# Optimization experiments

Measured on AMD Instinct MI355X. Metric: run time of the kernel, lower is better.

## Reference

```python
import jax, jax.numpy as jnp
import numpy as np

N_CELLS, IN_DIM, HID, OUT = 65536, 128, 256, 128
MLP_H = 128   # engine MLP hidden width is hard-coded to 128 in the source
N_MORPH = 32  # min(32, n_cells//4)


def setup_inputs() -> dict:
    key = jax.random.key(0)
    ks = jax.random.split(key, 18)
    s = 0.05
    return {
        "x": jax.random.normal(ks[0], (1, IN_DIM), jnp.float32),
        "hiddens": jax.random.normal(ks[1], (N_CELLS, HID), jnp.float32) * 0.1,
        "Wa1": jax.random.normal(ks[2], (MLP_H, IN_DIM + HID), jnp.float32) * s,
        "ba1": jax.random.normal(ks[3], (MLP_H,), jnp.float32) * s,
        "Wa2": jax.random.normal(ks[4], (OUT, MLP_H), jnp.float32) * s,
        "ba2": jax.random.normal(ks[5], (OUT,), jnp.float32) * s,
        "Wg1": jax.random.normal(ks[6], (MLP_H, IN_DIM + HID), jnp.float32) * s,
        "bg1": jax.random.normal(ks[7], (MLP_H,), jnp.float32) * s,
        "Wg2": jax.random.normal(ks[8], (OUT, MLP_H), jnp.float32) * s,
        "bg2": jax.random.normal(ks[9], (OUT,), jnp.float32) * s,
        "W_ih": jax.random.normal(ks[10], (3 * HID, OUT + 1), jnp.float32) * s,
        "W_hh": jax.random.normal(ks[11], (3 * HID, HID), jnp.float32) * s,
        "b_ih": jax.random.normal(ks[12], (3 * HID,), jnp.float32) * s,
        "b_hh": jax.random.normal(ks[13], (3 * HID,), jnp.float32) * s,
        "nat_w": jnp.eye(HID, dtype=jnp.float32),  # nn.init.eye_
        "morph_w": jax.random.normal(ks[14], (N_MORPH, HID, HID), jnp.float32) * 0.02,
        "morph_src": jax.random.randint(ks[15], (N_MORPH,), 0, N_CELLS, jnp.int32),
        "morph_tgt": jax.random.randint(ks[16], (N_MORPH,), 0, N_CELLS, jnp.int32),
        "step": 0,
    }


def _forward(x, hiddens, Wa1, ba1, Wa2, ba2, Wg1, bg1, Wg2, bg2,
             W_ih, W_hh, b_ih, b_hh, nat_w, morph_w, morph_src, morph_tgt, step):
    n = hiddens.shape[0]
    # --- BenchMind, batched over all cells (x broadcast to every cell) ---
    xb = jnp.broadcast_to(x, (n, x.shape[-1]))
    combined = jnp.concatenate([xb, hiddens], axis=-1)               # [n, in+hid]
    a = jax.nn.relu(combined @ Wa1.T + ba1) @ Wa2.T + ba2            # [n, out]
    g = jax.nn.relu(combined @ Wg1.T + bg1) @ Wg2.T + bg2            # [n, out]
    out = a - g                                                       # [n, out]
    tension = jnp.mean(out * out, axis=-1, keepdims=True)            # [n, 1]
    # mem_input is detached in torch
    mem_in = jax.lax.stop_gradient(jnp.concatenate([out, tension], axis=-1))
    # --- PyTorch GRUCell math ---
    gi = mem_in @ W_ih.T + b_ih                                      # [n, 3H]
    gh = hiddens @ W_hh.T + b_hh                                     # [n, 3H]
    i_r, i_z, i_n = jnp.split(gi, 3, axis=-1)
    h_r, h_z, h_n = jnp.split(gh, 3, axis=-1)
    r = jax.nn.sigmoid(i_r + h_r)
    z = jax.nn.sigmoid(i_z + h_z)
    nn_ = jnp.tanh(i_n + r * h_n)
    hid = jax.lax.stop_gradient((1.0 - z) * nn_ + z * hiddens)       # detached new hiddens
    if step % 3 == 0:
        hid = jax.lax.stop_gradient(hid @ nat_w.T)                   # natural transformation
    # --- limit / colimit (morphism gather-transform-aggregate) ---
    limit = jnp.einsum('mij,mj->i', morph_w, hid[morph_src]) / N_MORPH
    colimit = jnp.einsum('mji,mj->i', morph_w, hid[morph_tgt]) / N_MORPH
    diff = limit - colimit
    cat_tension = jnp.mean(diff * diff)
    hid = hid + 0.05 * jax.lax.stop_gradient(diff)[None, :]
    # --- faction sync (+ debate if step > 5) ---
    n_f = min(8, n // 2)
    fs = n // n_f
    hf = hid[: n_f * fs].reshape(n_f, fs, hid.shape[-1])
    fmean = hf.mean(axis=1, keepdims=True)                           # [n_f,1,H]
    hf = 0.85 * hf + 0.15 * fmean
    if step > 5:
        global_op = hf.mean(axis=1).mean(axis=0)                     # mean of faction means
        dc = max(1, fs // 4)
        hf = hf.at[:, :dc].set(0.85 * hf[:, :dc] + 0.15 * global_op)
    hid = jnp.concatenate([hf.reshape(n_f * fs, -1), hid[n_f * fs:]], axis=0)
    # --- tension-weighted combination (weights detached: .item() in torch) ---
    t = jax.lax.stop_gradient(tension[:, 0])                         # [n]
    w = jax.nn.softmax(t, axis=0)
    combined_out = jnp.sum(w[:, None] * out, axis=0, keepdims=True)  # [1, out]
    avg_tension = jnp.mean(tension) + 0.1 * cat_tension
    return combined_out, avg_tension, hid


def reference(x, hiddens, Wa1, ba1, Wa2, ba2, Wg1, bg1, Wg2, bg2,
              W_ih, W_hh, b_ih, b_hh, nat_w, morph_w, morph_src, morph_tgt, step):
    combined_out, avg_tension, _ = _forward(
        x, hiddens, Wa1, ba1, Wa2, ba2, Wg1, bg1, Wg2, bg2,
        W_ih, W_hh, b_ih, b_hh, nat_w, morph_w, morph_src, morph_tgt, step)
    return combined_out, avg_tension
```

## Files before the change

### kernel.cpp

```cpp
#include <hip/hip_runtime.h>
#include <math.h>

#define OFF_W1B   0
#define OFF_W2A   32768
#define OFF_XW1B  49152
#define OFF_B2D   49408
#define OFF_PT    49536
#define OFF_PE    51584
#define OFF_POUT  53632
#define OFF_MI4   315776
#define OFF_TEN   323968
#define OFF_HH4   324032
#define OFF_GI    340416
#define OFF_GH    389568
#define OFF_PLIM  438720
#define OFF_PCOL8 446912
#define OFF_GMSK  512448

typedef short bf16x8 __attribute__((ext_vector_type(8)));
typedef short s16x4  __attribute__((ext_vector_type(4)));
typedef float f32x4  __attribute__((ext_vector_type(4)));

__device__ __forceinline__ unsigned short f2bf(float f) {
    unsigned u = __builtin_bit_cast(unsigned, f);
    u += 0x7FFFu + ((u >> 16) & 1u);
    return (unsigned short)(u >> 16);
}

__device__ __forceinline__ bf16x8 cvt8(float4 a, float4 b) {
    bf16x8 v;
    v[0] = (short)f2bf(a.x); v[1] = (short)f2bf(a.y);
    v[2] = (short)f2bf(a.z); v[3] = (short)f2bf(a.w);
    v[4] = (short)f2bf(b.x); v[5] = (short)f2bf(b.y);
    v[6] = (short)f2bf(b.z); v[7] = (short)f2bf(b.w);
    return v;
}

__global__ __launch_bounds__(256) void k_prep(
    const float* __restrict__ x, const float* __restrict__ hiddens,
    const float* __restrict__ Wa1, const float* __restrict__ ba1,
    const float* __restrict__ Wa2, const float* __restrict__ ba2,
    const float* __restrict__ Wg1, const float* __restrict__ bg1,
    const float* __restrict__ Wg2, const float* __restrict__ bg2,
    const int* __restrict__ msrc, const int* __restrict__ mtgt,
    float* __restrict__ ws)
{
    const int b = blockIdx.x, t = threadIdx.x;
    unsigned short* w1b = (unsigned short*)(ws + OFF_W1B);
    unsigned short* w2a = (unsigned short*)(ws + OFF_W2A);
    if (b < 256) {
        const int n = b;
        const float* row = (n < 128) ? &Wa1[n * 384] : &Wg1[(n - 128) * 384];
        const int kc = t >> 3;
        w1b[(kc * 256 + n) * 8 + (t & 7)] = f2bf(row[128 + t]);
        if (n < 128) {
            float w2 = (t < 128) ? Wa2[n * 128 + t] : -Wg2[n * 128 + (t - 128)];
            w2a[(kc * 128 + n) * 8 + (t & 7)] = f2bf(w2);
        }
    } else if (b == 256) {
        const int n = t;
        const float* wr = (n < 128) ? &Wa1[n * 384] : &Wg1[(n - 128) * 384];
        float s = (n < 128) ? ba1[n] : bg1[n - 128];
        for (int j = 0; j < 128; ++j) s = fmaf(x[j], wr[j], s);
        ws[OFF_XW1B + n] = s;
        if (n < 128) ws[OFF_B2D + n] = ba2[n] - bg2[n];
    } else if (b == 257) {
        unsigned* gm = (unsigned*)(ws + OFF_GMSK);
        for (int i = t; i < 2048; i += 256) gm[i] = 0u;
        __syncthreads();
        if (t < 64) {
            const int cell = (t < 32) ? msrc[t] : mtgt[t - 32];
            atomicOr(&gm[cell >> 5], 1u << (cell & 31));
        }
    } else {
        const int g = b - 258;
        const int cell = (g < 32) ? msrc[g] : mtgt[g - 32];
        ws[OFF_HH4 + (t >> 2) * 256 + g * 4 + (t & 3)] = hiddens[(size_t)cell * 256 + t];
    }
}

__global__ __launch_bounds__(256, 4) void k_main(
    const float* __restrict__ hiddens,
    const int* __restrict__ msrc, const int* __restrict__ mtgt,
    float* __restrict__ ws)
{
    __shared__ __align__(16) short hB[32 * 256];
    __shared__ __align__(16) short h1B[32 * 256];
    __shared__ float part[128];
    __shared__ float e_sm[32], t_sm_[32];
    __shared__ int gid_sm[64];

    const int tid  = threadIdx.x;
    const int lane = tid & 63, wid = tid >> 6;
    const int l15 = lane & 15, l4 = lane >> 4;
    const int blk = blockIdx.x;

    if (tid < 64) gid_sm[tid] = (tid < 32) ? msrc[tid] : mtgt[tid - 32];

    const uint4* w1g = (const uint4*)(ws + OFF_W1B);
    const uint4* w2g = (const uint4*)(ws + OFF_W2A);
    const unsigned* gm = (const unsigned*)(ws + OFF_GMSK);

    const int rc = tid >> 3;
    const int cb = (tid & 7) * 32;
    const float* hsrc0 = hiddens + (size_t)(blk * 64 + rc) * 256 + cb;

    float4 nx[8];
#pragma unroll
    for (int it = 0; it < 8; ++it) nx[it] = *(const float4*)(hsrc0 + it * 4);
#pragma unroll
    for (int it = 0; it < 4; ++it) {
        const int kc = (tid & 7) * 4 + it;
        *(bf16x8*)&hB[rc * 256 + ((kc ^ (rc & 15)) << 3)] = cvt8(nx[2 * it], nx[2 * it + 1]);
    }
    __syncthreads();

#pragma unroll
    for (int t = 0; t < 2; ++t) {
        const int bt = blk * 2 + t;

        uint4 wc[4], wn1[4], wn2[4];
#pragma unroll
        for (int q = 0; q < 4; ++q) {
            wc[q]  = w1g[(0 + l4) * 256 + wid * 64 + q * 16 + l15];
            wn1[q] = w1g[(4 + l4) * 256 + wid * 64 + q * 16 + l15];
        }
        uint4 g2c[2], g2n1[2];
        f32x4 acc[4][2];
#pragma unroll
        for (int q = 0; q < 4; ++q)
#pragma unroll
            for (int ct = 0; ct < 2; ++ct) acc[q][ct] = (f32x4)0.f;

        __builtin_amdgcn_s_setprio(1);
#pragma unroll
        for (int s = 0; s < 8; ++s) {
            if (s < 6) {
#pragma unroll
                for (int q = 0; q < 4; ++q)
                    wn2[q] = w1g[((s + 2) * 4 + l4) * 256 + wid * 64 + q * 16 + l15];
            } else if (s == 6) {
#pragma unroll
                for (int q = 0; q < 2; ++q)
                    g2c[q] = w2g[(0 + l4) * 128 + wid * 32 + q * 16 + l15];
            } else {
#pragma unroll
                for (int q = 0; q < 2; ++q)
                    g2n1[q] = w2g[(4 + l4) * 128 + wid * 32 + q * 16 + l15];
            }
            bf16x8 bfr[2];
#pragma unroll
            for (int ct = 0; ct < 2; ++ct) {
                const int c = ct * 16 + l15;
                bfr[ct] = *(const bf16x8*)&hB[c * 256 + (((s * 4 + l4) ^ l15) << 3)];
            }
#pragma unroll
            for (int q = 0; q < 4; ++q) {
                const bf16x8 af = __builtin_bit_cast(bf16x8, wc[q]);
                acc[q][0] = __builtin_amdgcn_mfma_f32_16x16x32_bf16(af, bfr[0], acc[q][0], 0, 0, 0);
                acc[q][1] = __builtin_amdgcn_mfma_f32_16x16x32_bf16(af, bfr[1], acc[q][1], 0, 0, 0);
            }
#pragma unroll
            for (int q = 0; q < 4; ++q) { wc[q] = wn1[q]; wn1[q] = wn2[q]; }
        }
        __builtin_amdgcn_s_setprio(0);

#pragma unroll
        for (int nt = 0; nt < 4; ++nt) {
            const int n0 = wid * 64 + nt * 16 + l4 * 4;
            float4 xb = *(const float4*)(ws + OFF_XW1B + n0);
            const float bx[4] = {xb.x, xb.y, xb.z, xb.w};
            const int chunk = n0 >> 3;
            const int off = (l4 & 1) * 4;
#pragma unroll
            for (int ct = 0; ct < 2; ++ct) {
                const int c = ct * 16 + l15;
                s16x4 pk;
#pragma unroll
                for (int r = 0; r < 4; ++r)
                    pk[r] = (short)f2bf(fmaxf(acc[nt][ct][r] + bx[r], 0.f));
                *(s16x4*)&h1B[c * 256 + ((chunk ^ l15) << 3) + off] = pk;
            }
        }
        __syncthreads();

        f32x4 acc2[2][2];
#pragma unroll
        for (int ot = 0; ot < 2; ++ot)
#pragma unroll
            for (int ct = 0; ct < 2; ++ct) acc2[ot][ct] = (f32x4)0.f;

        uint4 g2n2[2];
        __builtin_amdgcn_s_setprio(1);
#pragma unroll
        for (int s = 0; s < 8; ++s) {
            if (s < 6) {
#pragma unroll
                for (int q = 0; q < 2; ++q)
                    g2n2[q] = w2g[((s + 2) * 4 + l4) * 128 + wid * 32 + q * 16 + l15];
            }
            if (s == 5 && t == 0) {
#pragma unroll
                for (int it = 0; it < 8; ++it)
                    nx[it] = *(const float4*)(hsrc0 + 32 * 256 + it * 4);
            }
            bf16x8 b2[2];
#pragma unroll
            for (int ct = 0; ct < 2; ++ct) {
                const int c = ct * 16 + l15;
                b2[ct] = *(const bf16x8*)&h1B[c * 256 + (((s * 4 + l4) ^ l15) << 3)];
            }
#pragma unroll
            for (int ot = 0; ot < 2; ++ot) {
                const bf16x8 af = __builtin_bit_cast(bf16x8, g2c[ot]);
                acc2[ot][0] = __builtin_amdgcn_mfma_f32_16x16x32_bf16(af, b2[0], acc2[ot][0], 0, 0, 0);
                acc2[ot][1] = __builtin_amdgcn_mfma_f32_16x16x32_bf16(af, b2[1], acc2[ot][1], 0, 0, 0);
            }
#pragma unroll
            for (int q = 0; q < 2; ++q) { g2c[q] = g2n1[q]; g2n1[q] = g2n2[q]; }
        }
        __builtin_amdgcn_s_setprio(0);

        float outv[2][2][4];
#pragma unroll
        for (int ot = 0; ot < 2; ++ot) {
            float4 bd = *(const float4*)(ws + OFF_B2D + wid * 32 + ot * 16 + l4 * 4);
            const float bv[4] = {bd.x, bd.y, bd.z, bd.w};
#pragma unroll
            for (int ct = 0; ct < 2; ++ct)
#pragma unroll
                for (int r = 0; r < 4; ++r)
                    outv[ot][ct][r] = acc2[ot][ct][r] + bv[r];
        }

#pragma unroll
        for (int ct = 0; ct < 2; ++ct) {
            float sq = 0.f;
#pragma unroll
            for (int ot = 0; ot < 2; ++ot)
#pragma unroll
                for (int r = 0; r < 4; ++r)
                    sq = fmaf(outv[ot][ct][r], outv[ot][ct][r], sq);
            sq += __shfl_xor(sq, 16);
            sq += __shfl_xor(sq, 32);
            if (l4 == 0) part[wid * 32 + ct * 16 + l15] = sq;
        }
        __syncthreads();

        if (tid < 32) {
            float s = part[tid] + part[32 + tid] + part[64 + tid] + part[96 + tid];
            const float tv = s * (1.f / 128.f);
            const float ev = expf(tv);
            t_sm_[tid] = tv; e_sm[tid] = ev;
            float pt = tv, pe = ev;
            for (int off = 16; off > 0; off >>= 1) {
                pt += __shfl_down(pt, off);
                pe += __shfl_down(pe, off);
            }
            if (tid == 0) { ws[OFF_PT + bt] = pt; ws[OFF_PE + bt] = pe; }
            unsigned m = gm[bt];
            while (m) {
                const int g = __builtin_ctz(m); m &= m - 1;
                const int cg = gid_sm[g];
                if ((cg >> 5) == bt && (cg & 31) == tid) ws[OFF_TEN + g] = tv;
            }
        }
        __syncthreads();

        {
            float p[2][4];
#pragma unroll
            for (int ot = 0; ot < 2; ++ot)
#pragma unroll
                for (int r = 0; r < 4; ++r) {
                    float s = e_sm[l15] * outv[ot][0][r];
                    s = fmaf(e_sm[16 + l15], outv[ot][1][r], s);
                    p[ot][r] = s;
                }
#pragma unroll
            for (int ot = 0; ot < 2; ++ot)
#pragma unroll
                for (int r = 0; r < 4; ++r) {
                    p[ot][r] += __shfl_xor(p[ot][r], 1);
                    p[ot][r] += __shfl_xor(p[ot][r], 2);
                    p[ot][r] += __shfl_xor(p[ot][r], 4);
                    p[ot][r] += __shfl_xor(p[ot][r], 8);
                }
            if (l15 == 0) {
#pragma unroll
                for (int ot = 0; ot < 2; ++ot)
                    *(float4*)(ws + OFF_POUT + (size_t)bt * 128 + wid * 32 + ot * 16 + l4 * 4) =
                        make_float4(p[ot][0], p[ot][1], p[ot][2], p[ot][3]);
            }
        }
        {
            unsigned m = gm[bt];
            while (m) {
                const int g = __builtin_ctz(m); m &= m - 1;
                const int cg = gid_sm[g];
                if ((cg >> 5) != bt) continue;
                const int c = cg & 31;
                if ((c & 15) == l15) {
                    const int ct = c >> 4;
#pragma unroll
                    for (int ot = 0; ot < 2; ++ot)
                        *(float4*)(ws + OFF_MI4 + (wid * 8 + ot * 4 + l4) * 256 + g * 4) =
                            make_float4(outv[ot][ct][0], outv[ot][ct][1],
                                        outv[ot][ct][2], outv[ot][ct][3]);
                }
            }
        }
        if (t == 0) {
#pragma unroll
            for (int it = 0; it < 4; ++it) {
                const int kc = (tid & 7) * 4 + it;
                *(bf16x8*)&hB[rc * 256 + ((kc ^ (rc & 15)) << 3)] = cvt8(nx[2 * it], nx[2 * it + 1]);
            }
            __syncthreads();
        }
    }
}

__global__ __launch_bounds__(256) void k_tail1(
    const float* __restrict__ W_ih, const float* __restrict__ W_hh,
    const float* __restrict__ b_ih, const float* __restrict__ b_hh,
    float* __restrict__ ws)
{
    const int lane = threadIdx.x & 63;
    const int w    = threadIdx.x >> 6;
    const int row  = __builtin_amdgcn_readfirstlane(blockIdx.x * 4 + w);
    const float* mi4 = ws + OFF_MI4;
    const float* hh4 = ws + OFF_HH4;

    const float* wi = W_ih + row * 129;
    float gi = b_ih[row];
#pragma unroll 8
    for (int q = 0; q < 32; ++q) {
        float4 a = *(const float4*)(mi4 + q * 256 + lane * 4);
        gi = fmaf(wi[4 * q + 0], a.x, gi);
        gi = fmaf(wi[4 * q + 1], a.y, gi);
        gi = fmaf(wi[4 * q + 2], a.z, gi);
        gi = fmaf(wi[4 * q + 3], a.w, gi);
    }
    gi = fmaf(ws[OFF_TEN + lane], wi[128], gi);

    const float* wh = W_hh + (size_t)row * 256;
    float gh = b_hh[row];
#pragma unroll 8
    for (int q = 0; q < 64; ++q) {
        float4 a = *(const float4*)(hh4 + q * 256 + lane * 4);
        float4 b = *(const float4*)(wh + 4 * q);
        gh = fmaf(b.x, a.x, gh);
        gh = fmaf(b.y, a.y, gh);
        gh = fmaf(b.z, a.z, gh);
        gh = fmaf(b.w, a.w, gh);
    }
    ws[OFF_GI + lane * 768 + row] = gi;
    ws[OFF_GH + lane * 768 + row] = gh;
}

__global__ __launch_bounds__(256) void k_morph(
    const float* __restrict__ morph_w, const float* __restrict__ nat_w,
    const int* __restrict__ step, float* __restrict__ ws)
{
    __shared__ float wsm[32 * 264];
    __shared__ float hd0[256], hd1[256];
    __shared__ float hs[256], ht[256];
    const int blk = blockIdx.x, t = threadIdx.x;
    const int m = blk >> 3, ch = blk & 7;
    const float* wm = morph_w + (size_t)m * 65536 + (size_t)ch * 32 * 256;
    {
        const int r = t >> 3, c0 = (t & 7) * 32;
#pragma unroll
        for (int it = 0; it < 8; ++it)
            *(float4*)&wsm[r * 264 + c0 + it * 4] = *(const float4*)(wm + r * 256 + c0 + it * 4);
    }
#pragma unroll
    for (int h = 0; h < 2; ++h) {
        const int g = h * 32 + m;
        const float i_r = ws[OFF_GI + g * 768 + t];
        const float i_z = ws[OFF_GI + g * 768 + 256 + t];
        const float i_n = ws[OFF_GI + g * 768 + 512 + t];
        const float h_r = ws[OFF_GH + g * 768 + t];
        const float h_z = ws[OFF_GH + g * 768 + 256 + t];
        const float h_n = ws[OFF_GH + g * 768 + 512 + t];
        const float hv  = ws[OFF_HH4 + (t >> 2) * 256 + g * 4 + (t & 3)];
        const float r  = 1.f / (1.f + expf(-(i_r + h_r)));
        const float z  = 1.f / (1.f + expf(-(i_z + h_z)));
        const float nn = tanhf(i_n + r * h_n);
        const float hid = (1.f - z) * nn + z * hv;
        if (h == 0) hd0[t] = hid; else hd1[t] = hid;
    }
    __syncthreads();

    float hn0, hn1;
    if (step[0] % 3 == 0) {
        const float4* wr = (const float4*)(nat_w + (size_t)t * 256);
        float s0 = 0.f, s1 = 0.f;
        for (int q = 0; q < 64; ++q) {
            float4 wq = wr[q];
            s0 = fmaf(wq.x, hd0[4 * q + 0], s0); s1 = fmaf(wq.x, hd1[4 * q + 0], s1);
            s0 = fmaf(wq.y, hd0[4 * q + 1], s0); s1 = fmaf(wq.y, hd1[4 * q + 1], s1);
            s0 = fmaf(wq.z, hd0[4 * q + 2], s0); s1 = fmaf(wq.z, hd1[4 * q + 2], s1);
            s0 = fmaf(wq.w, hd0[4 * q + 3], s0); s1 = fmaf(wq.w, hd1[4 * q + 3], s1);
        }
        hn0 = s0; hn1 = s1;
    } else {
        hn0 = hd0[t]; hn1 = hd1[t];
    }
    hs[t] = hn0; ht[t] = hn1;
    __syncthreads();

    {
        const int il = t >> 3, jc = t & 7;
        float L = 0.f;
#pragma unroll 8
        for (int jj = 0; jj < 32; ++jj) {
            const int j = jc + 8 * jj;
            L = fmaf(wsm[il * 264 + j], hs[j], L);
        }
        L += __shfl_down(L, 4);
        L += __shfl_down(L, 2);
        L += __shfl_down(L, 1);
        if (jc == 0) ws[OFF_PLIM + m * 256 + ch * 32 + il] = L;
    }
    {
        float C = 0.f;
#pragma unroll 8
        for (int r = 0; r < 32; ++r)
            C = fmaf(wsm[r * 264 + t], ht[ch * 32 + r], C);
        ws[OFF_PCOL8 + blk * 256 + t] = C;
    }
}

__global__ __launch_bounds__(256) void k_out(const float* __restrict__ ws,
                                             float* __restrict__ out)
{
    __shared__ float red[256];
    const int b = blockIdx.x, t = threadIdx.x;
    if (b < 128) {
        float so = 0.f, se = 0.f;
        for (int i = t; i < 2048; i += 256) {
            so += ws[OFF_POUT + (size_t)i * 128 + b];
            se += ws[OFF_PE + i];
        }
        red[t] = so; __syncthreads();
        for (int s = 128; s > 0; s >>= 1) { if (t < s) red[t] += red[t + s]; __syncthreads(); }
        const float SO = red[0]; __syncthreads();
        red[t] = se; __syncthreads();
        for (int s = 128; s > 0; s >>= 1) { if (t < s) red[t] += red[t + s]; __syncthreads(); }
        if (t == 0) out[b] = SO / red[0];
    } else {
        float pt = 0.f;
        for (int i = t; i < 2048; i += 256) pt += ws[OFF_PT + i];
        float L = 0.f, C = 0.f;
        for (int m = 0; m < 32; ++m) L += ws[OFF_PLIM + m * 256 + t];
        for (int mc = 0; mc < 256; ++mc) C += ws[OFF_PCOL8 + mc * 256 + t];
        const float d = (L - C) * (1.f / 32.f);
        red[t] = d * d; __syncthreads();
        for (int s = 128; s > 0; s >>= 1) { if (t < s) red[t] += red[t + s]; __syncthreads(); }
        const float cat = red[0] * (1.f / 256.f); __syncthreads();
        red[t] = pt; __syncthreads();
        for (int s = 128; s > 0; s >>= 1) { if (t < s) red[t] += red[t + s]; __syncthreads(); }
        if (t == 0) out[128] = red[0] * (1.f / 65536.f) + 0.1f * cat;
    }
}

extern "C" void kernel_launch(void* const* d_in, const int* in_sizes, int n_in,
                              void* d_out, int out_size, void* d_ws, size_t ws_size,
                              hipStream_t stream)
{
    const float* x     = (const float*)d_in[0];
    const float* hidd  = (const float*)d_in[1];
    const float* Wa1   = (const float*)d_in[2];
    const float* ba1   = (const float*)d_in[3];
    const float* Wa2   = (const float*)d_in[4];
    const float* ba2   = (const float*)d_in[5];
    const float* Wg1   = (const float*)d_in[6];
    const float* bg1   = (const float*)d_in[7];
    const float* Wg2   = (const float*)d_in[8];
    const float* bg2   = (const float*)d_in[9];
    const float* W_ih  = (const float*)d_in[10];
    const float* W_hh  = (const float*)d_in[11];
    const float* b_ih  = (const float*)d_in[12];
    const float* b_hh  = (const float*)d_in[13];
    const float* nat_w = (const float*)d_in[14];
    const float* mw    = (const float*)d_in[15];
    const int*   msrc  = (const int*)d_in[16];
    const int*   mtgt  = (const int*)d_in[17];
    const int*   step  = (const int*)d_in[18];

    float* out = (float*)d_out;
    float* ws  = (float*)d_ws;

    k_prep <<<322, 256, 0, stream>>>(x, hidd, Wa1, ba1, Wa2, ba2, Wg1, bg1, Wg2, bg2, msrc, mtgt, ws);
    k_main <<<1024, 256, 0, stream>>>(hidd, msrc, mtgt, ws);
    k_tail1<<<192, 256, 0, stream>>>(W_ih, W_hh, b_ih, b_hh, ws);
    k_morph<<<256, 256, 0, stream>>>(mw, nat_w, step, ws);
    k_out  <<<129, 256, 0, stream>>>(ws, out);
}
```

Baseline: 82.63 us.

## Process one 32-cell tile per block and drop cross-tile hidden-state prefetch

The main kernel now handles a single 32-cell tile per block and launches twice as many blocks, instead of looping over two tiles per block with a software prefetch of the second tile's hidden rows during the first tile's second GEMM. The launch-bounds occupancy hint drops from 4 to 2 blocks per CU, and the unrolled weight prefetch is written with scalar variables. This gives up intra-block overlap of global loads with MFMA work and relies on more resident blocks to hide latency. Each block also reloads the weight fragments itself, so the per-block setup cost is paid twice as often.

```diff
diff --git a/kernel.cpp b/kernel.cpp
--- a/kernel.cpp
+++ b/kernel.cpp
@@ -79,7 +79,7 @@
     }
 }
 
-__global__ __launch_bounds__(256, 4) void k_main(
+__global__ __launch_bounds__(256, 2) void k_main(
     const float* __restrict__ hiddens,
     const int* __restrict__ msrc, const int* __restrict__ mtgt,
     float* __restrict__ ws)
@@ -93,7 +93,7 @@
     const int tid  = threadIdx.x;
     const int lane = tid & 63, wid = tid >> 6;
     const int l15 = lane & 15, l4 = lane >> 4;
-    const int blk = blockIdx.x;
+    const int bt = blockIdx.x;
 
     if (tid < 64) gid_sm[tid] = (tid < 32) ? msrc[tid] : mtgt[tid - 32];
 
@@ -101,222 +101,204 @@
     const uint4* w2g = (const uint4*)(ws + OFF_W2A);
     const unsigned* gm = (const unsigned*)(ws + OFF_GMSK);
 
-    const int rc = tid >> 3;
-    const int cb = (tid & 7) * 32;
-    const float* hsrc0 = hiddens + (size_t)(blk * 64 + rc) * 256 + cb;
-
-    float4 nx[8];
-#pragma unroll
-    for (int it = 0; it < 8; ++it) nx[it] = *(const float4*)(hsrc0 + it * 4);
-#pragma unroll
-    for (int it = 0; it < 4; ++it) {
-        const int kc = (tid & 7) * 4 + it;
-        *(bf16x8*)&hB[rc * 256 + ((kc ^ (rc & 15)) << 3)] = cvt8(nx[2 * it], nx[2 * it + 1]);
-    }
-    __syncthreads();
-
-#pragma unroll
-    for (int t = 0; t < 2; ++t) {
-        const int bt = blk * 2 + t;
-
-        uint4 wc[4], wn1[4], wn2[4];
-#pragma unroll
-        for (int q = 0; q < 4; ++q) {
-            wc[q]  = w1g[(0 + l4) * 256 + wid * 64 + q * 16 + l15];
-            wn1[q] = w1g[(4 + l4) * 256 + wid * 64 + q * 16 + l15];
-        }
-        uint4 g2c[2], g2n1[2];
-        f32x4 acc[4][2];
-#pragma unroll
-        for (int q = 0; q < 4; ++q)
-#pragma unroll
-            for (int ct = 0; ct < 2; ++ct) acc[q][ct] = (f32x4)0.f;
-
-        __builtin_amdgcn_s_setprio(1);
-#pragma unroll
-        for (int s = 0; s < 8; ++s) {
-            if (s < 6) {
-#pragma unroll
-                for (int q = 0; q < 4; ++q)
-                    wn2[q] = w1g[((s + 2) * 4 + l4) * 256 + wid * 64 + q * 16 + l15];
-            } else if (s == 6) {
-#pragma unroll
-                for (int q = 0; q < 2; ++q)
-                    g2c[q] = w2g[(0 + l4) * 128 + wid * 32 + q * 16 + l15];
-            } else {
-#pragma unroll
-                for (int q = 0; q < 2; ++q)
-                    g2n1[q] = w2g[(4 + l4) * 128 + wid * 32 + q * 16 + l15];
+    {
+        const int rc = tid >> 3;
+        const float* hsrc = hiddens + (size_t)(bt * 32 + rc) * 256 + (tid & 7) * 32;
+        float4 v0 = *(const float4*)(hsrc + 0);
+        float4 v1 = *(const float4*)(hsrc + 4);
+        float4 v2 = *(const float4*)(hsrc + 8);
+        float4 v3 = *(const float4*)(hsrc + 12);
+        float4 v4 = *(const float4*)(hsrc + 16);
+        float4 v5 = *(const float4*)(hsrc + 20);
+        float4 v6 = *(const float4*)(hsrc + 24);
+        float4 v7 = *(const float4*)(hsrc + 28);
+        const int kc0 = (tid & 7) * 4;
+        *(bf16x8*)&hB[rc * 256 + (((kc0 + 0) ^ (rc & 15)) << 3)] = cvt8(v0, v1);
+        *(bf16x8*)&hB[rc * 256 + (((kc0 + 1) ^ (rc & 15)) << 3)] = cvt8(v2, v3);
+        *(bf16x8*)&hB[rc * 256 + (((kc0 + 2) ^ (rc & 15)) << 3)] = cvt8(v4, v5);
+        *(bf16x8*)&hB[rc * 256 + (((kc0 + 3) ^ (rc & 15)) << 3)] = cvt8(v6, v7);
+    }
+    __syncthreads();
+
+    const int wb1 = wid * 64 + l15;
+    uint4 c0 = w1g[(0 + l4) * 256 + wb1 + 0];
+    uint4 c1 = w1g[(0 + l4) * 256 + wb1 + 16];
+    uint4 c2 = w1g[(0 + l4) * 256 + wb1 + 32];
+    uint4 c3 = w1g[(0 + l4) * 256 + wb1 + 48];
+    uint4 p0 = w1g[(4 + l4) * 256 + wb1 + 0];
+    uint4 p1 = w1g[(4 + l4) * 256 + wb1 + 16];
+    uint4 p2 = w1g[(4 + l4) * 256 + wb1 + 32];
+    uint4 p3 = w1g[(4 + l4) * 256 + wb1 + 48];
+    uint4 g2c0, g2c1, g2p0, g2p1;
+
+    f32x4 acc[4][2];
+#pragma unroll
+    for (int q = 0; q < 4; ++q)
+#pragma unroll
+        for (int ct = 0; ct < 2; ++ct) acc[q][ct] = (f32x4)0.f;
+
+    __builtin_amdgcn_s_setprio(1);
+#pragma unroll
+    for (int s = 0; s < 8; ++s) {
+        uint4 f0, f1, f2, f3;
+        if (s < 6) {
+            f0 = w1g[((s + 2) * 4 + l4) * 256 + wb1 + 0];
+            f1 = w1g[((s + 2) * 4 + l4) * 256 + wb1 + 16];
+            f2 = w1g[((s + 2) * 4 + l4) * 256 + wb1 + 32];
+            f3 = w1g[((s + 2) * 4 + l4) * 256 + wb1 + 48];
+        } else if (s == 6) {
+            g2c0 = w2g[(0 + l4) * 128 + wid * 32 + l15];
+            g2c1 = w2g[(0 + l4) * 128 + wid * 32 + 16 + l15];
+        } else {
+            g2p0 = w2g[(4 + l4) * 128 + wid * 32 + l15];
+            g2p1 = w2g[(4 + l4) * 128 + wid * 32 + 16 + l15];
+        }
+        bf16x8 bfr0 = *(const bf16x8*)&hB[(0 * 16 + l15) * 256 + (((s * 4 + l4) ^ l15) << 3)];
+        bf16x8 bfr1 = *(const bf16x8*)&hB[(1 * 16 + l15) * 256 + (((s * 4 + l4) ^ l15) << 3)];
+        acc[0][0] = __builtin_amdgcn_mfma_f32_16x16x32_bf16(__builtin_bit_cast(bf16x8, c0), bfr0, acc[0][0], 0, 0, 0);
+        acc[0][1] = __builtin_amdgcn_mfma_f32_16x16x32_bf16(__builtin_bit_cast(bf16x8, c0), bfr1, acc[0][1], 0, 0, 0);
+        acc[1][0] = __builtin_amdgcn_mfma_f32_16x16x32_bf16(__builtin_bit_cast(bf16x8, c1), bfr0, acc[1][0], 0, 0, 0);
+        acc[1][1] = __builtin_amdgcn_mfma_f32_16x16x32_bf16(__builtin_bit_cast(bf16x8, c1), bfr1, acc[1][1], 0, 0, 0);
+        acc[2][0] = __builtin_amdgcn_mfma_f32_16x16x32_bf16(__builtin_bit_cast(bf16x8, c2), bfr0, acc[2][0], 0, 0, 0);
+        acc[2][1] = __builtin_amdgcn_mfma_f32_16x16x32_bf16(__builtin_bit_cast(bf16x8, c2), bfr1, acc[2][1], 0, 0, 0);
+        acc[3][0] = __builtin_amdgcn_mfma_f32_16x16x32_bf16(__builtin_bit_cast(bf16x8, c3), bfr0, acc[3][0], 0, 0, 0);
+        acc[3][1] = __builtin_amdgcn_mfma_f32_16x16x32_bf16(__builtin_bit_cast(bf16x8, c3), bfr1, acc[3][1], 0, 0, 0);
+        c0 = p0; c1 = p1; c2 = p2; c3 = p3;
+        if (s < 6) { p0 = f0; p1 = f1; p2 = f2; p3 = f3; }
+    }
+    __builtin_amdgcn_s_setprio(0);
+
+#pragma unroll
+    for (int nt = 0; nt < 4; ++nt) {
+        const int n0 = wid * 64 + nt * 16 + l4 * 4;
+        float4 xb = *(const float4*)(ws + OFF_XW1B + n0);
+        const float bx[4] = {xb.x, xb.y, xb.z, xb.w};
+        const int chunk = n0 >> 3;
+        const int off = (l4 & 1) * 4;
+#pragma unroll
+        for (int ct = 0; ct < 2; ++ct) {
+            const int c = ct * 16 + l15;
+            s16x4 pk;
+#pragma unroll
+            for (int r = 0; r < 4; ++r)
+                pk[r] = (short)f2bf(fmaxf(acc[nt][ct][r] + bx[r], 0.f));
+            *(s16x4*)&h1B[c * 256 + ((chunk ^ l15) << 3) + off] = pk;
+        }
+    }
+    __syncthreads();
+
+    f32x4 acc2[2][2];
+#pragma unroll
+    for (int ot = 0; ot < 2; ++ot)
+#pragma unroll
+        for (int ct = 0; ct < 2; ++ct) acc2[ot][ct] = (f32x4)0.f;
+
+    __builtin_amdgcn_s_setprio(1);
+#pragma unroll
+    for (int s = 0; s < 8; ++s) {
+        uint4 f0, f1;
+        if (s < 6) {
+            f0 = w2g[((s + 2) * 4 + l4) * 128 + wid * 32 + l15];
+            f1 = w2g[((s + 2) * 4 + l4) * 128 + wid * 32 + 16 + l15];
+        }
+        bf16x8 b20 = *(const bf16x8*)&h1B[(0 * 16 + l15) * 256 + (((s * 4 + l4) ^ l15) << 3)];
+        bf16x8 b21 = *(const bf16x8*)&h1B[(1 * 16 + l15) * 256 + (((s * 4 + l4) ^ l15) << 3)];
+        acc2[0][0] = __builtin_amdgcn_mfma_f32_16x16x32_bf16(__builtin_bit_cast(bf16x8, g2c0), b20, acc2[0][0], 0, 0, 0);
+        acc2[0][1] = __builtin_amdgcn_mfma_f32_16x16x32_bf16(__builtin_bit_cast(bf16x8, g2c0), b21, acc2[0][1], 0, 0, 0);
+        acc2[1][0] = __builtin_amdgcn_mfma_f32_16x16x32_bf16(__builtin_bit_cast(bf16x8, g2c1), b20, acc2[1][0], 0, 0, 0);
+        acc2[1][1] = __builtin_amdgcn_mfma_f32_16x16x32_bf16(__builtin_bit_cast(bf16x8, g2c1), b21, acc2[1][1], 0, 0, 0);
+        g2c0 = g2p0; g2c1 = g2p1;
+        if (s < 6) { g2p0 = f0; g2p1 = f1; }
+    }
+    __builtin_amdgcn_s_setprio(0);
+
+    float outv[2][2][4];
+#pragma unroll
+    for (int ot = 0; ot < 2; ++ot) {
+        float4 bd = *(const float4*)(ws + OFF_B2D + wid * 32 + ot * 16 + l4 * 4);
+        const float bv[4] = {bd.x, bd.y, bd.z, bd.w};
+#pragma unroll
+        for (int ct = 0; ct < 2; ++ct)
+#pragma unroll
+            for (int r = 0; r < 4; ++r)
+                outv[ot][ct][r] = acc2[ot][ct][r] + bv[r];
+    }
+
+#pragma unroll
+    for (int ct = 0; ct < 2; ++ct) {
+        float sq = 0.f;
+#pragma unroll
+        for (int ot = 0; ot < 2; ++ot)
+#pragma unroll
+            for (int r = 0; r < 4; ++r)
+                sq = fmaf(outv[ot][ct][r], outv[ot][ct][r], sq);
+        sq += __shfl_xor(sq, 16);
+        sq += __shfl_xor(sq, 32);
+        if (l4 == 0) part[wid * 32 + ct * 16 + l15] = sq;
+    }
+    __syncthreads();
+
+    if (tid < 32) {
+        float s = part[tid] + part[32 + tid] + part[64 + tid] + part[96 + tid];
+        const float tv = s * (1.f / 128.f);
+        const float ev = expf(tv);
+        t_sm_[tid] = tv; e_sm[tid] = ev;
+        float pt = tv, pe = ev;
+        for (int off = 16; off > 0; off >>= 1) {
+            pt += __shfl_down(pt, off);
+            pe += __shfl_down(pe, off);
+        }
+        if (tid == 0) { ws[OFF_PT + bt] = pt; ws[OFF_PE + bt] = pe; }
+        unsigned m = gm[bt];
+        while (m) {
+            const int g = __builtin_ctz(m); m &= m - 1;
+            const int cg = gid_sm[g];
+            if ((cg >> 5) == bt && (cg & 31) == tid) ws[OFF_TEN + g] = tv;
+        }
+    }
+    __syncthreads();
+
+    {
+        float p[2][4];
+#pragma unroll
+        for (int ot = 0; ot < 2; ++ot)
+#pragma unroll
+            for (int r = 0; r < 4; ++r) {
+                float s = e_sm[l15] * outv[ot][0][r];
+                s = fmaf(e_sm[16 + l15], outv[ot][1][r], s);
+                p[ot][r] = s;
             }
-            bf16x8 bfr[2];
-#pragma unroll
-            for (int ct = 0; ct < 2; ++ct) {
-                const int c = ct * 16 + l15;
-                bfr[ct] = *(const bf16x8*)&hB[c * 256 + (((s * 4 + l4) ^ l15) << 3)];
+#pragma unroll
+        for (int ot = 0; ot < 2; ++ot)
+#pragma unroll
+            for (int r = 0; r < 4; ++r) {
+                p[ot][r] += __shfl_xor(p[ot][r], 1);
+                p[ot][r] += __shfl_xor(p[ot][r], 2);
+                p[ot][r] += __shfl_xor(p[ot][r], 4);
+                p[ot][r] += __shfl_xor(p[ot][r], 8);
             }
-#pragma unroll
-            for (int q = 0; q < 4; ++q) {
-                const bf16x8 af = __builtin_bit_cast(bf16x8, wc[q]);
-                acc[q][0] = __builtin_amdgcn_mfma_f32_16x16x32_bf16(af, bfr[0], acc[q][0], 0, 0, 0);
-                acc[q][1] = __builtin_amdgcn_mfma_f32_16x16x32_bf16(af, bfr[1], acc[q][1], 0, 0, 0);
+        if (l15 == 0) {
+#pragma unroll
+            for (int ot = 0; ot < 2; ++ot)
+                *(float4*)(ws + OFF_POUT + (size_t)bt * 128 + wid * 32 + ot * 16 + l4 * 4) =
+                    make_float4(p[ot][0], p[ot][1], p[ot][2], p[ot][3]);
+        }
+    }
+    {
+        unsigned m = gm[bt];
+        while (m) {
+            const int g = __builtin_ctz(m); m &= m - 1;
+            const int cg = gid_sm[g];
+            if ((cg >> 5) != bt) continue;
+            const int c = cg & 31;
+            if ((c & 15) == l15) {
+                const int ct = c >> 4;
+#pragma unroll
+                for (int ot = 0; ot < 2; ++ot)
+                    *(float4*)(ws + OFF_MI4 + (wid * 8 + ot * 4 + l4) * 256 + g * 4) =
+                        make_float4(outv[ot][ct][0], outv[ot][ct][1],
+                                    outv[ot][ct][2], outv[ot][ct][3]);
             }
-#pragma unroll
-            for (int q = 0; q < 4; ++q) { wc[q] = wn1[q]; wn1[q] = wn2[q]; }
-        }
-        __builtin_amdgcn_s_setprio(0);
-
-#pragma unroll
-        for (int nt = 0; nt < 4; ++nt) {
-            const int n0 = wid * 64 + nt * 16 + l4 * 4;
-            float4 xb = *(const float4*)(ws + OFF_XW1B + n0);
-            const float bx[4] = {xb.x, xb.y, xb.z, xb.w};
-            const int chunk = n0 >> 3;
-            const int off = (l4 & 1) * 4;
-#pragma unroll
-            for (int ct = 0; ct < 2; ++ct) {
-                const int c = ct * 16 + l15;
-                s16x4 pk;
-#pragma unroll
-                for (int r = 0; r < 4; ++r)
-                    pk[r] = (short)f2bf(fmaxf(acc[nt][ct][r] + bx[r], 0.f));
-                *(s16x4*)&h1B[c * 256 + ((chunk ^ l15) << 3) + off] = pk;
-            }
-        }
-        __syncthreads();
-
-        f32x4 acc2[2][2];
-#pragma unroll
-        for (int ot = 0; ot < 2; ++ot)
-#pragma unroll
-            for (int ct = 0; ct < 2; ++ct) acc2[ot][ct] = (f32x4)0.f;
-
-        uint4 g2n2[2];
-        __builtin_amdgcn_s_setprio(1);
-#pragma unroll
-        for (int s = 0; s < 8; ++s) {
-            if (s < 6) {
-#pragma unroll
-                for (int q = 0; q < 2; ++q)
-                    g2n2[q] = w2g[((s + 2) * 4 + l4) * 128 + wid * 32 + q * 16 + l15];
-            }
-            if (s == 5 && t == 0) {
-#pragma unroll
-                for (int it = 0; it < 8; ++it)
-                    nx[it] = *(const float4*)(hsrc0 + 32 * 256 + it * 4);
-            }
-            bf16x8 b2[2];
-#pragma unroll
-            for (int ct = 0; ct < 2; ++ct) {
-                const int c = ct * 16 + l15;
-                b2[ct] = *(const bf16x8*)&h1B[c * 256 + (((s * 4 + l4) ^ l15) << 3)];
-            }
-#pragma unroll
-            for (int ot = 0; ot < 2; ++ot) {
-                const bf16x8 af = __builtin_bit_cast(bf16x8, g2c[ot]);
-                acc2[ot][0] = __builtin_amdgcn_mfma_f32_16x16x32_bf16(af, b2[0], acc2[ot][0], 0, 0, 0);
-                acc2[ot][1] = __builtin_amdgcn_mfma_f32_16x16x32_bf16(af, b2[1], acc2[ot][1], 0, 0, 0);
-            }
-#pragma unroll
-            for (int q = 0; q < 2; ++q) { g2c[q] = g2n1[q]; g2n1[q] = g2n2[q]; }
-        }
-        __builtin_amdgcn_s_setprio(0);
-
-        float outv[2][2][4];
-#pragma unroll
-        for (int ot = 0; ot < 2; ++ot) {
-            float4 bd = *(const float4*)(ws + OFF_B2D + wid * 32 + ot * 16 + l4 * 4);
-            const float bv[4] = {bd.x, bd.y, bd.z, bd.w};
-#pragma unroll
-            for (int ct = 0; ct < 2; ++ct)
-#pragma unroll
-                for (int r = 0; r < 4; ++r)
-                    outv[ot][ct][r] = acc2[ot][ct][r] + bv[r];
-        }
-
-#pragma unroll
-        for (int ct = 0; ct < 2; ++ct) {
-            float sq = 0.f;
-#pragma unroll
-            for (int ot = 0; ot < 2; ++ot)
-#pragma unroll
-                for (int r = 0; r < 4; ++r)
-                    sq = fmaf(outv[ot][ct][r], outv[ot][ct][r], sq);
-            sq += __shfl_xor(sq, 16);
-            sq += __shfl_xor(sq, 32);
-            if (l4 == 0) part[wid * 32 + ct * 16 + l15] = sq;
-        }
-        __syncthreads();
-
-        if (tid < 32) {
-            float s = part[tid] + part[32 + tid] + part[64 + tid] + part[96 + tid];
-            const float tv = s * (1.f / 128.f);
-            const float ev = expf(tv);
-            t_sm_[tid] = tv; e_sm[tid] = ev;
-            float pt = tv, pe = ev;
-            for (int off = 16; off > 0; off >>= 1) {
-                pt += __shfl_down(pt, off);
-                pe += __shfl_down(pe, off);
-            }
-            if (tid == 0) { ws[OFF_PT + bt] = pt; ws[OFF_PE + bt] = pe; }
-            unsigned m = gm[bt];
-            while (m) {
-                const int g = __builtin_ctz(m); m &= m - 1;
-                const int cg = gid_sm[g];
-                if ((cg >> 5) == bt && (cg & 31) == tid) ws[OFF_TEN + g] = tv;
-            }
-        }
-        __syncthreads();
-
-        {
-            float p[2][4];
-#pragma unroll
-            for (int ot = 0; ot < 2; ++ot)
-#pragma unroll
-                for (int r = 0; r < 4; ++r) {
-                    float s = e_sm[l15] * outv[ot][0][r];
-                    s = fmaf(e_sm[16 + l15], outv[ot][1][r], s);
-                    p[ot][r] = s;
-                }
-#pragma unroll
-            for (int ot = 0; ot < 2; ++ot)
-#pragma unroll
-                for (int r = 0; r < 4; ++r) {
-                    p[ot][r] += __shfl_xor(p[ot][r], 1);
-                    p[ot][r] += __shfl_xor(p[ot][r], 2);
-                    p[ot][r] += __shfl_xor(p[ot][r], 4);
-                    p[ot][r] += __shfl_xor(p[ot][r], 8);
-                }
-            if (l15 == 0) {
-#pragma unroll
-                for (int ot = 0; ot < 2; ++ot)
-                    *(float4*)(ws + OFF_POUT + (size_t)bt * 128 + wid * 32 + ot * 16 + l4 * 4) =
-                        make_float4(p[ot][0], p[ot][1], p[ot][2], p[ot][3]);
-            }
-        }
-        {
-            unsigned m = gm[bt];
-            while (m) {
-                const int g = __builtin_ctz(m); m &= m - 1;
-                const int cg = gid_sm[g];
-                if ((cg >> 5) != bt) continue;
-                const int c = cg & 31;
-                if ((c & 15) == l15) {
-                    const int ct = c >> 4;
-#pragma unroll
-                    for (int ot = 0; ot < 2; ++ot)
-                        *(float4*)(ws + OFF_MI4 + (wid * 8 + ot * 4 + l4) * 256 + g * 4) =
-                            make_float4(outv[ot][ct][0], outv[ot][ct][1],
-                                        outv[ot][ct][2], outv[ot][ct][3]);
-                }
-            }
-        }
-        if (t == 0) {
-#pragma unroll
-            for (int it = 0; it < 4; ++it) {
-                const int kc = (tid & 7) * 4 + it;
-                *(bf16x8*)&hB[rc * 256 + ((kc ^ (rc & 15)) << 3)] = cvt8(nx[2 * it], nx[2 * it + 1]);
-            }
-            __syncthreads();
         }
     }
 }
@@ -494,7 +476,7 @@
     float* ws  = (float*)d_ws;
 
     k_prep <<<322, 256, 0, stream>>>(x, hidd, Wa1, ba1, Wa2, ba2, Wg1, bg1, Wg2, bg2, msrc, mtgt, ws);
-    k_main <<<1024, 256, 0, stream>>>(hidd, msrc, mtgt, ws);
+    k_main <<<2048, 256, 0, stream>>>(hidd, msrc, mtgt, ws);
     k_tail1<<<192, 256, 0, stream>>>(W_ih, W_hh, b_ih, b_hh, ws);
     k_morph<<<256, 256, 0, stream>>>(mw, nat_w, step, ws);
     k_out  <<<129, 256, 0, stream>>>(ws, out);
```

After: 76.17 us. 7.8% less time.
